# Optimization experiments

Hardware: AMD Instinct MI355X
Metric: run time of the kernel (lower is better)

The kernel has to match this reference:

```python
import jax, jax.numpy as jnp
from jax import lax
import numpy as np

C_IN, C_OUT, G, K, PAD = 64, 128, 4, 3, 1
P = K * K
CG = C_IN // G
N, H, W = 8, 64, 64
LN_EPS = 1e-6
BN_EPS = 1e-5


def setup_inputs() -> dict:
    key = jax.random.key(0)
    ks = jax.random.split(key, 32)
    r = lambda i, shape, s=0.05: jax.random.normal(ks[i], shape, dtype=jnp.float32) * s
    return dict(
        x=jax.random.normal(ks[0], (N, C_IN, H, W), dtype=jnp.float32),
        reflectance=jax.random.uniform(ks[1], (N, 1, H, W), dtype=jnp.float32),
        gain_w1=r(2, (C_IN, C_IN // 4)), gain_b1=r(3, (C_IN // 4,)),
        gain_w2=r(4, (C_IN // 4, C_IN)), gain_b2=r(5, (C_IN,)),
        tap_w=r(6, (C_IN,)), tap_b=r(7, (C_IN,)),
        dw_w=r(8, (K, K, 1, C_IN)), dw_b=r(9, (C_IN,)),
        ln_g=jnp.ones((C_IN,), jnp.float32), ln_b=jnp.zeros((C_IN,), jnp.float32),
        inp_w=r(10, (C_IN, C_IN)), inp_b=r(11, (C_IN,)),
        off_w=r(12, (C_IN, G * P * 2), 0.02), off_b=r(13, (G * P * 2,), 0.02),
        mask_w=r(14, (C_IN, G * P), 0.02), mask_b=r(15, (G * P,), 0.02),
        outp_w=r(16, (C_IN, C_IN)), outp_b=r(17, (C_IN,)),
        conv_w=r(18, (C_IN, C_OUT)), conv_b=r(19, (C_OUT,)),
        bn1_g=jnp.ones((C_IN,), jnp.float32), bn1_b=jnp.zeros((C_IN,), jnp.float32),
        bn1_m=r(20, (C_IN,)),
        bn1_v=jax.random.uniform(ks[21], (C_IN,), minval=0.5, maxval=1.5),
        bn2_g=jnp.ones((C_OUT,), jnp.float32), bn2_b=jnp.zeros((C_OUT,), jnp.float32),
        bn2_m=r(22, (C_OUT,)),
        bn2_v=jax.random.uniform(ks[23], (C_OUT,), minval=0.5, maxval=1.5),
    )


def _bilinear_gather(xg, py, px):
    # xg: (N, Hp, Wp, G, CG); py/px: (N, H, W, G, P) absolute pixel coords
    # replicates F.grid_sample(mode='bilinear', padding_mode='zeros', align_corners=False)
    n_, Hp, Wp = xg.shape[0], xg.shape[1], xg.shape[2]
    y0 = jnp.floor(py)
    x0 = jnp.floor(px)
    wy = py - y0
    wx = px - x0
    nI = jnp.arange(n_).reshape(n_, 1, 1, 1, 1)
    gI = jnp.arange(G).reshape(1, 1, 1, G, 1)
    out = jnp.zeros(py.shape + (CG,), xg.dtype)
    for dy in (0, 1):
        for dx in (0, 1):
            yi = y0 + dy
            xi = x0 + dx
            w = (wy if dy else 1.0 - wy) * (wx if dx else 1.0 - wx)
            valid = (yi >= 0) & (yi < Hp) & (xi >= 0) & (xi < Wp)
            yc = jnp.clip(yi, 0, Hp - 1).astype(jnp.int32)
            xc = jnp.clip(xi, 0, Wp - 1).astype(jnp.int32)
            v = xg[nI, yc, xc, gI]  # (N, H, W, G, P, CG)
            out = out + (w * valid.astype(w.dtype))[..., None] * v
    return out


def reference(x, reflectance, gain_w1, gain_b1, gain_w2, gain_b2, tap_w, tap_b,
              dw_w, dw_b, ln_g, ln_b, inp_w, inp_b, off_w, off_b, mask_w, mask_b,
              outp_w, outp_b, conv_w, conv_b, bn1_g, bn1_b, bn1_m, bn1_v,
              bn2_g, bn2_b, bn2_m, bn2_v):
    n_, c_, h_, w_ = x.shape
    # ---- GainBlock (SE-style): x * sigmoid(mlp(avgpool(x))) + x ----
    pooled = x.mean(axis=(2, 3))                               # (N, C)
    g = jax.nn.relu(pooled @ gain_w1 + gain_b1)
    gain = jax.nn.sigmoid(g @ gain_w2 + gain_b2)               # (N, C)
    x = x * gain[:, :, None, None] + x
    # ---- ReflectiveFeedback: x + relu(conv1x1(reflectance)) ----
    refl = jax.nn.relu(reflectance * tap_w[None, :, None, None] + tap_b[None, :, None, None])
    x = x + refl                                               # (N, C, H, W)
    # ---- DCNv3 (pytorch version, group=4, k=3, pad=1, stride=1) ----
    xh = jnp.transpose(x, (0, 2, 3, 1))                        # NHWC
    xp = xh @ inp_w + inp_b                                    # input_proj
    dw = lax.conv_general_dilated(xh, dw_w, (1, 1), 'SAME',
                                  feature_group_count=c_,
                                  dimension_numbers=('NHWC', 'HWIO', 'NHWC')) + dw_b
    mu = dw.mean(-1, keepdims=True)
    var = dw.var(-1, keepdims=True)
    dw = ln_g * (dw - mu) * lax.rsqrt(var + LN_EPS) + ln_b     # LN channels_last
    dw = jax.nn.gelu(dw, approximate=False)
    offset = (dw @ off_w + off_b).reshape(n_, h_, w_, G, P, 2)
    mask = jax.nn.softmax((dw @ mask_w + mask_b).reshape(n_, h_, w_, G, P), axis=-1)
    # dcnv3_core: pad input, build reference + dilation grids (normalized by padded size)
    xpad = jnp.pad(xp, ((0, 0), (PAD, PAD), (PAD, PAD), (0, 0)))
    Hp, Wp = h_ + 2 * PAD, w_ + 2 * PAD
    ctr = (K - 1) // 2  # = (dilation*(k-1))//2 with dilation=1
    ref_y = (jnp.arange(h_, dtype=jnp.float32) + ctr + 0.5) / Hp
    ref_x = (jnp.arange(w_, dtype=jnp.float32) + ctr + 0.5) / Wp
    kk = jnp.arange(K, dtype=jnp.float32) - ctr                # [-1, 0, 1]
    gx = jnp.repeat(kk, K) / Wp                                # w-outer, h-inner order
    gy = jnp.tile(kk, K) / Hp
    loc_x = (ref_x[None, None, :, None, None] + gx[None, None, None, None, :]
             + offset[..., 0] / Wp)                            # (N,H,W,G,P)
    loc_y = (ref_y[None, :, None, None, None] + gy[None, None, None, None, :]
             + offset[..., 1] / Hp)
    px = loc_x * Wp - 0.5   # align_corners=False pixel coords
    py = loc_y * Hp - 0.5
    xg = xpad.reshape(n_, Hp, Wp, G, CG)
    samp = _bilinear_gather(xg, py, px)                        # (N,H,W,G,P,CG)
    dcn = (samp * mask[..., None]).sum(axis=4).reshape(n_, h_, w_, c_)
    dcn = dcn @ outp_w + outp_b                                # output_proj
    y = jnp.transpose(dcn, (0, 3, 1, 2))                       # back to NCHW
    # ---- bn1 -> relu -> conv1x1 -> bn2 -> relu (eval-mode BN) ----
    y = bn1_g[None, :, None, None] * (y - bn1_m[None, :, None, None]) \
        * lax.rsqrt(bn1_v[None, :, None, None] + BN_EPS) + bn1_b[None, :, None, None]
    y = jax.nn.relu(y)
    y = jnp.einsum('nchw,cd->ndhw', y, conv_w) + conv_b[None, :, None, None]
    y = bn2_g[None, :, None, None] * (y - bn2_m[None, :, None, None]) \
        * lax.rsqrt(bn2_v[None, :, None, None] + BN_EPS) + bn2_b[None, :, None, None]
    return jax.nn.relu(y)
```

## Files before the change

kernel.cpp:

```cpp
#include <hip/hip_runtime.h>
#include <math.h>


__global__ __launch_bounds__(256) void k_pool(const float* x, float* pooled) {
    __shared__ float red[256];
    int b = blockIdx.x;
    int nc = ((b & 7) << 6) | (b >> 3);
    const float4* p4 = reinterpret_cast<const float4*>(x + (size_t)nc * 4096);
    float s = 0.f;
    for (int i = threadIdx.x; i < 1024; i += 256) {
        float4 v = p4[i];
        s += v.x + v.y + v.z + v.w;
    }
    red[threadIdx.x] = s;
    __syncthreads();
    for (int o = 128; o > 0; o >>= 1) {
        if (threadIdx.x < o) red[threadIdx.x] += red[threadIdx.x + o];
        __syncthreads();
    }
    if (threadIdx.x == 0) pooled[nc] = red[0] * (1.f / 4096.f);
}

__global__ __launch_bounds__(256) void k_xsproj(
        const float* x, const float* refl,
        const float* tap_w, const float* tap_b,
        const float* pooled,
        const float* gw1, const float* gb1,
        const float* gw2, const float* gb2,
        const float* inp_w, const float* inp_b,
        float* xs, float* xpad) {
    __shared__ float tile[64 * 17];
    __shared__ float xsrow[16][68];
    __shared__ float hid[16];
    __shared__ float gain[64];
    __shared__ float rrow[16];
    int b = blockIdx.x;
    int n = b & 7, rem = b >> 3;
    int h = rem >> 2, wc = rem & 3, w0 = wc * 16;
    int nh = n * 64 + h;
    int tid = threadIdx.x;

    {
        int c = tid >> 2, wq = (tid & 3) * 4;
        const float4 v = *reinterpret_cast<const float4*>(
            &x[(((size_t)(n * 64 + c)) * 64 + h) * 64 + w0 + wq]);
        tile[c * 17 + wq + 0] = v.x;
        tile[c * 17 + wq + 1] = v.y;
        tile[c * 17 + wq + 2] = v.z;
        tile[c * 17 + wq + 3] = v.w;
    }
    if (tid < 16) rrow[tid] = refl[n * 4096 + h * 64 + w0 + tid];
    if (tid >= 64 && tid < 80) {
        int j = tid - 64;
        float s = gb1[j];
        for (int c = 0; c < 64; ++c) s += pooled[n * 64 + c] * gw1[c * 16 + j];
        hid[j] = fmaxf(s, 0.f);
    }
    __syncthreads();

    if (tid < 64) {
        float s = gb2[tid];
        #pragma unroll
        for (int j = 0; j < 16; ++j) s += hid[j] * gw2[j * 64 + tid];
        gain[tid] = 1.f + 1.f / (1.f + expf(-s));
    }
    __syncthreads();

    {
        int c = tid & 63, wbq = tid >> 6;
        float gv = gain[c], tw = tap_w[c], tb = tap_b[c];
        #pragma unroll
        for (int k = 0; k < 4; ++k) {
            int w = wbq + k * 4;
            float r = fmaxf(rrow[w] * tw + tb, 0.f);
            float v = tile[c * 17 + w] * gv + r;
            xsrow[w][c] = v;
            xs[(((size_t)nh) * 64 + w0 + w) * 64 + c] = v;
        }
    }
    __syncthreads();

    {
        int co = tid & 63, wg = tid >> 6;
        float acc[4];
        float bv = inp_b[co];
        #pragma unroll
        for (int i = 0; i < 4; ++i) acc[i] = bv;
        for (int c4 = 0; c4 < 64; c4 += 4) {
            float q0 = inp_w[(c4 + 0) * 64 + co];
            float q1 = inp_w[(c4 + 1) * 64 + co];
            float q2 = inp_w[(c4 + 2) * 64 + co];
            float q3 = inp_w[(c4 + 3) * 64 + co];
            #pragma unroll
            for (int i = 0; i < 4; ++i) {
                float4 d = *reinterpret_cast<const float4*>(&xsrow[wg * 4 + i][c4]);
                acc[i] += d.x * q0 + d.y * q1 + d.z * q2 + d.w * q3;
            }
        }
        const size_t rowb = (((size_t)n * 66) + (h + 1)) * 66;
        #pragma unroll
        for (int i = 0; i < 4; ++i) {
            int w = wg * 4 + i;
            xpad[(rowb + (w0 + w + 1)) * 64 + co] = acc[i];
        }
        if (wc == 0 && tid < 64) xpad[rowb * 64 + tid] = 0.f;
        if (wc == 3 && tid < 64) xpad[(rowb + 65) * 64 + tid] = 0.f;
        if (h == 0 || h == 63) {
            const size_t rb = (((size_t)n * 66) + (h == 0 ? 0 : 65)) * 66;
            for (int i = tid; i < 1024; i += 256) {
                int q = 1 + w0 + (i >> 6), cc = i & 63;
                xpad[(rb + q) * 64 + cc] = 0.f;
            }
            if (wc == 0 && tid < 64) xpad[rb * 64 + tid] = 0.f;
            if (wc == 3 && tid < 64) xpad[(rb + 65) * 64 + tid] = 0.f;
        }
    }
}

__global__ __launch_bounds__(128) void k_dwsamp(const float* xs, const float* xpad,
                       const float* dw_w, const float* dw_b,
                       const float* ln_g, const float* ln_b,
                       const float* off_w, const float* off_b,
                       const float* mask_w, const float* mask_b,
                       const float* outp_w, const float* outp_b,
                       const float* bn1_g, const float* bn1_b,
                       const float* bn1_m, const float* bn1_v,
                       float* vbuf) {
    __shared__ float  dwr[8][64];
    __shared__ float  mlog[8][40];
    __shared__ int4   sad[8][36];
    __shared__ float4 swt[8][36];
    __shared__ float  dcnl[8][64];

    int tid = threadIdx.x;
    int lane = tid & 63, wv = tid >> 6;
    int b = blockIdx.x;
    int n = b & 7;
    int pos0 = (b >> 3) * 8 + wv * 4;
    int h = pos0 >> 6, w0 = pos0 & 63;
    int lbase = wv * 4;
    int pbase = n * 4096 + pos0;

    {
        float dwk[9];
        #pragma unroll
        for (int k = 0; k < 9; ++k) dwk[k] = dw_w[k * 64 + lane];
        float s[4];
        float bvv = dw_b[lane];
        #pragma unroll
        for (int p = 0; p < 4; ++p) s[p] = bvv;
        for (int ky = 0; ky < 3; ++ky) {
            int y = h + ky - 1;
            if (y < 0 || y > 63) continue;
            const float* xrow = xs + ((size_t)(n * 64 + y)) * 4096;
            float v[6];
            #pragma unroll
            for (int dx = 0; dx < 6; ++dx) {
                int x2 = w0 - 1 + dx;
                v[dx] = (x2 >= 0 && x2 <= 63) ? xrow[x2 * 64 + lane] : 0.f;
            }
            float k0 = dwk[ky * 3 + 0], k1 = dwk[ky * 3 + 1], k2 = dwk[ky * 3 + 2];
            #pragma unroll
            for (int p = 0; p < 4; ++p)
                s[p] += v[p] * k0 + v[p + 1] * k1 + v[p + 2] * k2;
        }
        float lngv = ln_g[lane], lnbv = ln_b[lane];
        #pragma unroll
        for (int p = 0; p < 4; ++p) {
            float sv = s[p];
            float sum = sv, sq = sv * sv;
            #pragma unroll
            for (int o = 32; o > 0; o >>= 1) {
                sum += __shfl_xor(sum, o, 64);
                sq  += __shfl_xor(sq,  o, 64);
            }
            float mu = sum * (1.f / 64.f);
            float var = sq * (1.f / 64.f) - mu * mu;
            float nrm = (sv - mu) * rsqrtf(var + 1e-6f) * lngv + lnbv;
            dwr[lbase + p][lane] = 0.5f * nrm * (1.f + erff(nrm * 0.70710678118654752f));
        }
    }
    __syncthreads();

    float a0[4], a1[4];
    {
        int jb = lane * 2;
        const float* wptr;
        int stride;
        float b0 = 0.f, b1 = 0.f;
        if (lane < 36)      { wptr = off_w + jb;         stride = 72; b0 = off_b[jb];       b1 = off_b[jb + 1]; }
        else if (lane < 54) { wptr = mask_w + (jb - 72); stride = 36; b0 = mask_b[jb - 72]; b1 = mask_b[jb - 71]; }
        else                { wptr = off_w;              stride = 0; }
        #pragma unroll
        for (int p = 0; p < 4; ++p) { a0[p] = b0; a1[p] = b1; }
        for (int c4 = 0; c4 < 64; c4 += 4) {
            float4 d0 = *reinterpret_cast<const float4*>(&dwr[lbase + 0][c4]);
            float4 d1 = *reinterpret_cast<const float4*>(&dwr[lbase + 1][c4]);
            float4 d2 = *reinterpret_cast<const float4*>(&dwr[lbase + 2][c4]);
            float4 d3 = *reinterpret_cast<const float4*>(&dwr[lbase + 3][c4]);
            float dk0[4] = {d0.x, d0.y, d0.z, d0.w};
            float dk1[4] = {d1.x, d1.y, d1.z, d1.w};
            float dk2[4] = {d2.x, d2.y, d2.z, d2.w};
            float dk3[4] = {d3.x, d3.y, d3.z, d3.w};
            #pragma unroll
            for (int k = 0; k < 4; ++k) {
                float2 w2 = *reinterpret_cast<const float2*>(wptr);
                wptr += stride;
                a0[0] += dk0[k] * w2.x;  a1[0] += dk0[k] * w2.y;
                a0[1] += dk1[k] * w2.x;  a1[1] += dk1[k] * w2.y;
                a0[2] += dk2[k] * w2.x;  a1[2] += dk2[k] * w2.y;
                a0[3] += dk3[k] * w2.x;  a1[3] += dk3[k] * w2.y;
            }
        }
        if (lane >= 36 && lane < 54) {
            int jm = lane * 2 - 72;
            #pragma unroll
            for (int p = 0; p < 4; ++p) {
                mlog[lbase + p][jm]     = a0[p];
                mlog[lbase + p][jm + 1] = a1[p];
            }
        }
    }
    __syncthreads();

    if (lane < 36) {
        int g = lane / 9, pp = lane - g * 9;
        #pragma unroll
        for (int p = 0; p < 4; ++p) {
            int li = lbase + p;
            const float* lrow = &mlog[li][g * 9];
            float m = lrow[0];
            #pragma unroll
            for (int k = 1; k < 9; ++k) m = fmaxf(m, lrow[k]);
            float ssum = 0.f, ek = 0.f;
            #pragma unroll
            for (int k = 0; k < 9; ++k) {
                float e = expf(lrow[k] - m);
                ssum += e;
                if (k == pp) ek = e;
            }
            float mk = ek / ssum;
            float px = (float)((w0 + p) + (pp / 3)) + a0[p];
            float py = (float)(h + (pp % 3)) + a1[p];
            float x0f = floorf(px), y0f = floorf(py);
            float wx = px - x0f, wy = py - y0f;
            int x0 = (int)x0f, y0 = (int)y0f;
            int x1 = x0 + 1, y1 = y0 + 1;
            int xc0 = min(max(x0, 0), 65), xc1 = min(max(x1, 0), 65);
            int yc0 = min(max(y0, 0), 65), yc1 = min(max(y1, 0), 65);
            float vx0 = (x0 >= 0 && x0 < 66) ? 1.f : 0.f;
            float vx1 = (x1 >= 0 && x1 < 66) ? 1.f : 0.f;
            float vy0 = (y0 >= 0 && y0 < 66) ? 1.f : 0.f;
            float vy1 = (y1 >= 0 && y1 < 66) ? 1.f : 0.f;
            float wx0 = (1.f - wx) * vx0, wx1 = wx * vx1;
            float wy0 = (1.f - wy) * vy0, wy1 = wy * vy1;
            swt[li][lane] = make_float4(mk * wy0 * wx0, mk * wy0 * wx1,
                                        mk * wy1 * wx0, mk * wy1 * wx1);
            sad[li][lane] = make_int4((yc0 * 66 + xc0) * 64, (yc0 * 66 + xc1) * 64,
                                      (yc1 * 66 + xc0) * 64, (yc1 * 66 + xc1) * 64);
        }
    }
    __syncthreads();

    {
        int gb = (lane >> 4) * 9;
        const float* xpn = xpad + (size_t)n * 66 * 66 * 64;
        #pragma unroll
        for (int p = 0; p < 4; ++p) {
            int li = lbase + p;
            float acc = 0.f;
            #pragma unroll
            for (int pp = 0; pp < 9; ++pp) {
                int4   a  = sad[li][gb + pp];
                float4 cw = swt[li][gb + pp];
                acc += cw.x * xpn[a.x + lane] + cw.y * xpn[a.y + lane]
                     + cw.z * xpn[a.z + lane] + cw.w * xpn[a.w + lane];
            }
            dcnl[li][lane] = acc;
        }
    }
    __syncthreads();

    {
        float ob = outp_b[lane];
        float s0 = ob, s1 = ob, s2 = ob, s3 = ob;
        for (int c4 = 0; c4 < 64; c4 += 4) {
            float w0v = outp_w[(c4 + 0) * 64 + lane];
            float w1v = outp_w[(c4 + 1) * 64 + lane];
            float w2v = outp_w[(c4 + 2) * 64 + lane];
            float w3v = outp_w[(c4 + 3) * 64 + lane];
            float4 d0 = *reinterpret_cast<const float4*>(&dcnl[lbase + 0][c4]);
            float4 d1 = *reinterpret_cast<const float4*>(&dcnl[lbase + 1][c4]);
            float4 d2 = *reinterpret_cast<const float4*>(&dcnl[lbase + 2][c4]);
            float4 d3 = *reinterpret_cast<const float4*>(&dcnl[lbase + 3][c4]);
            s0 += d0.x * w0v + d0.y * w1v + d0.z * w2v + d0.w * w3v;
            s1 += d1.x * w0v + d1.y * w1v + d1.z * w2v + d1.w * w3v;
            s2 += d2.x * w0v + d2.y * w1v + d2.z * w2v + d2.w * w3v;
            s3 += d3.x * w0v + d3.y * w1v + d3.z * w2v + d3.w * w3v;
        }
        float sc = bn1_g[lane] * rsqrtf(bn1_v[lane] + 1e-5f);
        float sh = bn1_b[lane] - sc * bn1_m[lane];
        vbuf[(size_t)(pbase + 0) * 64 + lane] = fmaxf(sc * s0 + sh, 0.f);
        vbuf[(size_t)(pbase + 1) * 64 + lane] = fmaxf(sc * s1 + sh, 0.f);
        vbuf[(size_t)(pbase + 2) * 64 + lane] = fmaxf(sc * s2 + sh, 0.f);
        vbuf[(size_t)(pbase + 3) * 64 + lane] = fmaxf(sc * s3 + sh, 0.f);
    }
}

__global__ __launch_bounds__(256) void k_out(const float* vbuf,
                      const float* conv_w, const float* conv_b,
                      const float* bn2_g, const float* bn2_b,
                      const float* bn2_m, const float* bn2_v,
                      float* out) {
    __shared__ float vl[64 * 68];
    int b = blockIdx.x;
    int n = b & 7, rem = b >> 3;
    int h = rem >> 1, dh = (rem & 1) * 64;
    int tid = threadIdx.x;
    const float4* vrow4 = reinterpret_cast<const float4*>(vbuf + ((size_t)(n * 64 + h)) * 4096);
    for (int i = tid; i < 1024; i += 256) {
        int idx = i * 4;
        int w = idx >> 6, c = idx & 63;
        *reinterpret_cast<float4*>(&vl[w * 68 + c]) = vrow4[i];
    }
    __syncthreads();

    int dgrp = tid & 15, wgrp = tid >> 4;
    int dbase = dgrp * 4, wbase = wgrp * 4;
    float acc[4][4];
    #pragma unroll
    for (int i = 0; i < 4; ++i)
        #pragma unroll
        for (int j = 0; j < 4; ++j) acc[i][j] = 0.f;

    for (int c = 0; c < 64; ++c) {
        float v0 = vl[(wbase + 0) * 68 + c];
        float v1 = vl[(wbase + 1) * 68 + c];
        float v2 = vl[(wbase + 2) * 68 + c];
        float v3 = vl[(wbase + 3) * 68 + c];
        float4 wA = *reinterpret_cast<const float4*>(&conv_w[c * 128 + dh + dbase]);
        float wt[4] = {wA.x, wA.y, wA.z, wA.w};
        #pragma unroll
        for (int j = 0; j < 4; ++j) {
            acc[0][j] += v0 * wt[j];
            acc[1][j] += v1 * wt[j];
            acc[2][j] += v2 * wt[j];
            acc[3][j] += v3 * wt[j];
        }
    }

    #pragma unroll
    for (int j = 0; j < 4; ++j) {
        int d = dh + dbase + j;
        float sc = bn2_g[d] * rsqrtf(bn2_v[d] + 1e-5f);
        float sh = sc * (conv_b[d] - bn2_m[d]) + bn2_b[d];
        float4 r;
        r.x = fmaxf(sc * acc[0][j] + sh, 0.f);
        r.y = fmaxf(sc * acc[1][j] + sh, 0.f);
        r.z = fmaxf(sc * acc[2][j] + sh, 0.f);
        r.w = fmaxf(sc * acc[3][j] + sh, 0.f);
        size_t o = (((size_t)(n * 128 + d)) * 64 + h) * 64 + wbase;
        *reinterpret_cast<float4*>(out + o) = r;
    }
}

extern "C" void kernel_launch(void* const* d_in, const int* in_sizes, int n_in,
                              void* d_out, int out_size, void* d_ws, size_t ws_size,
                              hipStream_t stream) {
    const float* x      = (const float*)d_in[0];
    const float* refl   = (const float*)d_in[1];
    const float* gw1    = (const float*)d_in[2];
    const float* gb1    = (const float*)d_in[3];
    const float* gw2    = (const float*)d_in[4];
    const float* gb2    = (const float*)d_in[5];
    const float* tap_w  = (const float*)d_in[6];
    const float* tap_b  = (const float*)d_in[7];
    const float* dw_w   = (const float*)d_in[8];
    const float* dw_b   = (const float*)d_in[9];
    const float* ln_g   = (const float*)d_in[10];
    const float* ln_b   = (const float*)d_in[11];
    const float* inp_w  = (const float*)d_in[12];
    const float* inp_b  = (const float*)d_in[13];
    const float* off_w  = (const float*)d_in[14];
    const float* off_b  = (const float*)d_in[15];
    const float* mask_w = (const float*)d_in[16];
    const float* mask_b = (const float*)d_in[17];
    const float* outp_w = (const float*)d_in[18];
    const float* outp_b = (const float*)d_in[19];
    const float* conv_w = (const float*)d_in[20];
    const float* conv_b = (const float*)d_in[21];
    const float* bn1_g  = (const float*)d_in[22];
    const float* bn1_b  = (const float*)d_in[23];
    const float* bn1_m  = (const float*)d_in[24];
    const float* bn1_v  = (const float*)d_in[25];
    const float* bn2_g  = (const float*)d_in[26];
    const float* bn2_b  = (const float*)d_in[27];
    const float* bn2_m  = (const float*)d_in[28];
    const float* bn2_v  = (const float*)d_in[29];

    float* ws     = (float*)d_ws;
    float* pooled = ws;
    float* xs     = ws + 512;
    float* xpad   = xs + 2097152;
    float* vbuf   = xpad + 2230272;

    k_pool<<<512, 256, 0, stream>>>(x, pooled);
    k_xsproj<<<2048, 256, 0, stream>>>(x, refl, tap_w, tap_b, pooled,
                                       gw1, gb1, gw2, gb2, inp_w, inp_b, xs, xpad);
    k_dwsamp<<<4096, 128, 0, stream>>>(xs, xpad, dw_w, dw_b, ln_g, ln_b,
                                       off_w, off_b, mask_w, mask_b,
                                       outp_w, outp_b, bn1_g, bn1_b, bn1_m, bn1_v, vbuf);
    k_out<<<1024, 256, 0, stream>>>(vbuf, conv_w, conv_b, bn2_g, bn2_b, bn2_m, bn2_v,
                                    (float*)d_out);
}
```

Measured before the change: 206.4 us.

## Fuse 1x1 conv, BN2 and ReLU into deformable sampling kernel

The separate k_out kernel is removed. Its 64->128 pointwise conv, BN2 and ReLU now run at the end of k_dwsamp, reading the BN1/ReLU activations from shared memory instead of a global vbuf round trip. This cuts one kernel launch and the write and re-read of the intermediate buffer. In exchange, each wave does more ALU work per position and issues scattered float4 stores across 128 channel planes. Softmax and gain exponentials also switch to the fast __expf intrinsic.

```diff
diff --git a/kernel.cpp b/kernel.cpp
--- a/kernel.cpp
+++ b/kernel.cpp
@@ -62,7 +62,7 @@
         float s = gb2[tid];
         #pragma unroll
         for (int j = 0; j < 16; ++j) s += hid[j] * gw2[j * 64 + tid];
-        gain[tid] = 1.f + 1.f / (1.f + expf(-s));
+        gain[tid] = 1.f + 1.f / (1.f + __expf(-s));
     }
     __syncthreads();
 
@@ -125,7 +125,10 @@
                        const float* outp_w, const float* outp_b,
                        const float* bn1_g, const float* bn1_b,
                        const float* bn1_m, const float* bn1_v,
-                       float* vbuf) {
+                       const float* conv_w, const float* conv_b,
+                       const float* bn2_g, const float* bn2_b,
+                       const float* bn2_m, const float* bn2_v,
+                       float* out) {
     __shared__ float  dwr[8][64];
     __shared__ float  mlog[8][40];
     __shared__ int4   sad[8][36];
@@ -139,7 +142,6 @@
     int pos0 = (b >> 3) * 8 + wv * 4;
     int h = pos0 >> 6, w0 = pos0 & 63;
     int lbase = wv * 4;
-    int pbase = n * 4096 + pos0;
 
     {
         float dwk[9];
@@ -235,7 +237,7 @@
             float ssum = 0.f, ek = 0.f;
             #pragma unroll
             for (int k = 0; k < 9; ++k) {
-                float e = expf(lrow[k] - m);
+                float e = __expf(lrow[k] - m);
                 ssum += e;
                 if (k == pp) ek = e;
             }
@@ -300,67 +302,53 @@
         }
         float sc = bn1_g[lane] * rsqrtf(bn1_v[lane] + 1e-5f);
         float sh = bn1_b[lane] - sc * bn1_m[lane];
-        vbuf[(size_t)(pbase + 0) * 64 + lane] = fmaxf(sc * s0 + sh, 0.f);
-        vbuf[(size_t)(pbase + 1) * 64 + lane] = fmaxf(sc * s1 + sh, 0.f);
-        vbuf[(size_t)(pbase + 2) * 64 + lane] = fmaxf(sc * s2 + sh, 0.f);
-        vbuf[(size_t)(pbase + 3) * 64 + lane] = fmaxf(sc * s3 + sh, 0.f);
-    }
-}
-
-__global__ __launch_bounds__(256) void k_out(const float* vbuf,
-                      const float* conv_w, const float* conv_b,
-                      const float* bn2_g, const float* bn2_b,
-                      const float* bn2_m, const float* bn2_v,
-                      float* out) {
-    __shared__ float vl[64 * 68];
-    int b = blockIdx.x;
-    int n = b & 7, rem = b >> 3;
-    int h = rem >> 1, dh = (rem & 1) * 64;
-    int tid = threadIdx.x;
-    const float4* vrow4 = reinterpret_cast<const float4*>(vbuf + ((size_t)(n * 64 + h)) * 4096);
-    for (int i = tid; i < 1024; i += 256) {
-        int idx = i * 4;
-        int w = idx >> 6, c = idx & 63;
-        *reinterpret_cast<float4*>(&vl[w * 68 + c]) = vrow4[i];
-    }
-    __syncthreads();
-
-    int dgrp = tid & 15, wgrp = tid >> 4;
-    int dbase = dgrp * 4, wbase = wgrp * 4;
-    float acc[4][4];
-    #pragma unroll
-    for (int i = 0; i < 4; ++i)
-        #pragma unroll
-        for (int j = 0; j < 4; ++j) acc[i][j] = 0.f;
-
-    for (int c = 0; c < 64; ++c) {
-        float v0 = vl[(wbase + 0) * 68 + c];
-        float v1 = vl[(wbase + 1) * 68 + c];
-        float v2 = vl[(wbase + 2) * 68 + c];
-        float v3 = vl[(wbase + 3) * 68 + c];
-        float4 wA = *reinterpret_cast<const float4*>(&conv_w[c * 128 + dh + dbase]);
-        float wt[4] = {wA.x, wA.y, wA.z, wA.w};
-        #pragma unroll
-        for (int j = 0; j < 4; ++j) {
-            acc[0][j] += v0 * wt[j];
-            acc[1][j] += v1 * wt[j];
-            acc[2][j] += v2 * wt[j];
-            acc[3][j] += v3 * wt[j];
-        }
-    }
-
-    #pragma unroll
-    for (int j = 0; j < 4; ++j) {
-        int d = dh + dbase + j;
-        float sc = bn2_g[d] * rsqrtf(bn2_v[d] + 1e-5f);
-        float sh = sc * (conv_b[d] - bn2_m[d]) + bn2_b[d];
-        float4 r;
-        r.x = fmaxf(sc * acc[0][j] + sh, 0.f);
-        r.y = fmaxf(sc * acc[1][j] + sh, 0.f);
-        r.z = fmaxf(sc * acc[2][j] + sh, 0.f);
-        r.w = fmaxf(sc * acc[3][j] + sh, 0.f);
-        size_t o = (((size_t)(n * 128 + d)) * 64 + h) * 64 + wbase;
-        *reinterpret_cast<float4*>(out + o) = r;
+        dcnl[lbase + 0][lane] = fmaxf(sc * s0 + sh, 0.f);
+        dcnl[lbase + 1][lane] = fmaxf(sc * s1 + sh, 0.f);
+        dcnl[lbase + 2][lane] = fmaxf(sc * s2 + sh, 0.f);
+        dcnl[lbase + 3][lane] = fmaxf(sc * s3 + sh, 0.f);
+    }
+
+    {
+        float accA[4], accB[4];
+        #pragma unroll
+        for (int p = 0; p < 4; ++p) { accA[p] = 0.f; accB[p] = 0.f; }
+        for (int c4 = 0; c4 < 64; c4 += 4) {
+            float4 d0 = *reinterpret_cast<const float4*>(&dcnl[lbase + 0][c4]);
+            float4 d1 = *reinterpret_cast<const float4*>(&dcnl[lbase + 1][c4]);
+            float4 d2 = *reinterpret_cast<const float4*>(&dcnl[lbase + 2][c4]);
+            float4 d3 = *reinterpret_cast<const float4*>(&dcnl[lbase + 3][c4]);
+            float dk0[4] = {d0.x, d0.y, d0.z, d0.w};
+            float dk1[4] = {d1.x, d1.y, d1.z, d1.w};
+            float dk2[4] = {d2.x, d2.y, d2.z, d2.w};
+            float dk3[4] = {d3.x, d3.y, d3.z, d3.w};
+            #pragma unroll
+            for (int k = 0; k < 4; ++k) {
+                float wa = conv_w[(c4 + k) * 128 + lane];
+                float wb = conv_w[(c4 + k) * 128 + 64 + lane];
+                accA[0] += dk0[k] * wa;  accB[0] += dk0[k] * wb;
+                accA[1] += dk1[k] * wa;  accB[1] += dk1[k] * wb;
+                accA[2] += dk2[k] * wa;  accB[2] += dk2[k] * wb;
+                accA[3] += dk3[k] * wa;  accB[3] += dk3[k] * wb;
+            }
+        }
+        int dA = lane, dB = lane + 64;
+        float scA = bn2_g[dA] * rsqrtf(bn2_v[dA] + 1e-5f);
+        float shA = scA * (conv_b[dA] - bn2_m[dA]) + bn2_b[dA];
+        float scB = bn2_g[dB] * rsqrtf(bn2_v[dB] + 1e-5f);
+        float shB = scB * (conv_b[dB] - bn2_m[dB]) + bn2_b[dB];
+        float4 rA, rB;
+        rA.x = fmaxf(scA * accA[0] + shA, 0.f);
+        rA.y = fmaxf(scA * accA[1] + shA, 0.f);
+        rA.z = fmaxf(scA * accA[2] + shA, 0.f);
+        rA.w = fmaxf(scA * accA[3] + shA, 0.f);
+        rB.x = fmaxf(scB * accB[0] + shB, 0.f);
+        rB.y = fmaxf(scB * accB[1] + shB, 0.f);
+        rB.z = fmaxf(scB * accB[2] + shB, 0.f);
+        rB.w = fmaxf(scB * accB[3] + shB, 0.f);
+        size_t oA = (((size_t)(n * 128 + dA)) * 64 + h) * 64 + w0;
+        size_t oB = (((size_t)(n * 128 + dB)) * 64 + h) * 64 + w0;
+        *reinterpret_cast<float4*>(out + oA) = rA;
+        *reinterpret_cast<float4*>(out + oB) = rB;
     }
 }
 
@@ -402,14 +390,13 @@
     float* pooled = ws;
     float* xs     = ws + 512;
     float* xpad   = xs + 2097152;
-    float* vbuf   = xpad + 2230272;
 
     k_pool<<<512, 256, 0, stream>>>(x, pooled);
     k_xsproj<<<2048, 256, 0, stream>>>(x, refl, tap_w, tap_b, pooled,
                                        gw1, gb1, gw2, gb2, inp_w, inp_b, xs, xpad);
     k_dwsamp<<<4096, 128, 0, stream>>>(xs, xpad, dw_w, dw_b, ln_g, ln_b,
                                        off_w, off_b, mask_w, mask_b,
-                                       outp_w, outp_b, bn1_g, bn1_b, bn1_m, bn1_v, vbuf);
-    k_out<<<1024, 256, 0, stream>>>(vbuf, conv_w, conv_b, bn2_g, bn2_b, bn2_m, bn2_v,
-                                    (float*)d_out);
+                                       outp_w, outp_b, bn1_g, bn1_b, bn1_m, bn1_v,
+                                       conv_w, conv_b, bn2_g, bn2_b, bn2_m, bn2_v,
+                                       (float*)d_out);
 }
```

New measurement: 191.8 us. 1.08x faster.
